# Kernel optimization log

Measured on AMD Instinct MI355X. Metric: run time of the kernel, lower is better.

## Reference

```python
import jax, jax.numpy as jnp
import numpy as np

N = 50000   # nodes
E = 600000  # edges / hyperedge incidences
D = 128     # node_in_dim
H = 128     # hidden_dim
TAU = 0.5
ALPHA = 0.5
LAM = 0.5

_PARAM_SHAPES = [('Wq0', (1, H)), ('bq0', (H,)), ('W0', (D, H)), ('b0', (H,)),
                 ('Whq0', (1, H)), ('bhq0', (H,)), ('Wh0', (D, H)), ('bh0', (H,)),
                 ('Wf0', (H, H)), ('bf0', (H,)), ('Wfh0', (H, H)), ('bfh0', (H,)),
                 ('aq0', (H,)), ('a0', (H,)), ('ahq0', (H,)), ('ah0', (H,)),
                 ('aq_', (H,)), ('a_', (H,)), ('ahq_', (H,)), ('ah_', (H,)),
                 ('Wlq', (1, H)), ('blq', (H,)), ('Wlf', (D, H)), ('blf', (H,)),
                 ('Wm1', (H, H)), ('bm1', (H,)), ('Wm2', (H, H)), ('bm2', (H,))]


def setup_inputs() -> dict:
    key = jax.random.key(0)
    ks = jax.random.split(key, 8 + len(_PARAM_SHAPES))
    inp = {}
    inp['feats'] = jax.random.normal(ks[0], (N, D), dtype=jnp.float32)
    inp['edge_index'] = jax.random.randint(ks[1], (2, E), 0, N).astype(jnp.int32)
    inp['edge_index_aug'] = jax.random.randint(ks[2], (2, E), 0, N).astype(jnp.int32)
    inp['pos'] = jax.random.randint(ks[3], (100,), 1, N).astype(jnp.int32)
    inp['q'] = 0
    for i, (nm, sh) in enumerate(_PARAM_SHAPES):
        inp[nm] = jax.random.normal(ks[4 + i], sh, dtype=jnp.float32) * 0.05
    return inp


def _forward(feats, Wq0, bq0, W0, b0, Whq0, bhq0, Wh0, bh0, Wf0, bf0, Wfh0, bfh0,
             aq0, a0, ahq0, ah0, aq_, a_, ahq_, ah_, Wlq, blq, Wlf, blf,
             Wm1, bm1, Wm2, bm2, edge_index, edge_index_aug, q, pos):
    # ---- GCNConv (PyG default: add self-loops + symmetric normalization) ----
    sl = jnp.arange(N, dtype=edge_index.dtype)
    src = jnp.concatenate([edge_index[0], sl])
    dst = jnp.concatenate([edge_index[1], sl])
    deg = jax.ops.segment_sum(jnp.ones(src.shape[0], jnp.float32), dst, num_segments=N)
    dinv = jax.lax.rsqrt(deg)  # deg >= 1 thanks to self-loops
    enorm = dinv[src] * dinv[dst]

    def gcn(x, W, b):
        xw = x @ W
        return jax.ops.segment_sum(xw[src] * enorm[:, None], dst, num_segments=N) + b

    # ---- HypergraphConv (PyG, no attention): X' = D^-1 H B^-1 H^T X W ----
    node = edge_index_aug[0]
    he = edge_index_aug[1]
    Be = jax.ops.segment_sum(jnp.ones((E,), jnp.float32), he, num_segments=N)
    Dn = jax.ops.segment_sum(jnp.ones((E,), jnp.float32), node, num_segments=N)
    Binv = jnp.where(Be > 0, 1.0 / Be, 0.0)
    Dninv = jnp.where(Dn > 0, 1.0 / Dn, 0.0)

    def hg(x, W, b):
        xw = x @ W
        me = jax.ops.segment_sum(xw[node], he, num_segments=N) * Binv[:, None]
        return jax.ops.segment_sum(me[he], node, num_segments=N) * Dninv[:, None] + b

    # ---- attention-weighted fusion of two views (softmax over 2 logits) ----
    def fuse(a, b, wa, wb):
        att = jax.nn.softmax(jnp.stack([a @ wa, b @ wb], axis=1), axis=1)  # [N,2]
        return att[:, 0:1] * a + att[:, 1:2] * b

    querys = jnp.zeros((N, 1), jnp.float32).at[q].set(1.0)
    hq = jax.nn.relu(gcn(querys, Wq0, bq0))
    h = jax.nn.relu(gcn(feats, W0, b0))
    hf = fuse(hq, h, aq0, a0)
    h_augq = jax.nn.relu(hg(querys, Whq0, bhq0))
    h_aug = jax.nn.relu(hg(feats, Wh0, bh0))
    h_augf = fuse(h_augq, h_aug, ahq0, ah0)
    querys2 = querys @ Wlq + blq
    feats2 = feats @ Wlf + blf
    hf_ = fuse(querys2, feats2, aq_, a_)
    hf = jax.nn.relu(hf + gcn(hf_, Wf0, bf0))
    hfh_ = fuse(querys2, feats2, ahq_, ah_)
    h_augf = jax.nn.relu(h_augf + hg(hfh_, Wfh0, bfh0))

    def mlp(x):
        return jax.nn.relu(x @ Wm1 + bm1) @ Wm2 + bm2

    z = mlp(hf)
    z_aug = mlp(h_augf)

    # ---- Contra loss ----
    def expcos(v, M):
        num = M @ v
        den = jnp.maximum(jnp.linalg.norm(M, axis=1) * jnp.linalg.norm(v), 1e-8)
        return jnp.exp(num / den / TAU)

    sim1 = expcos(z[q], z)
    sim_aug1 = expcos(z_aug[q], z_aug)
    sim2 = expcos(z[q], z_aug)
    sim_aug2 = expcos(z_aug[q], z)
    mask = jnp.zeros((N,), bool).at[pos].set(True).at[q].set(False)
    nmask = jnp.sum(mask).astype(jnp.float32)

    def nlm(s):  # mean over positives of -log(s_i / sum(s))
        r = jnp.log(jnp.sum(s)) - jnp.log(s)
        return jnp.sum(jnp.where(mask, r, 0.0)) / nmask

    loss_intra = 0.5 * (nlm(sim1) + nlm(sim_aug1))
    loss_inter = 0.5 * (nlm(sim2) + nlm(sim_aug2))
    z_unsup = jnp.log(jnp.sum(sim2)) - jnp.log(sim2[q])
    z_aug_unsup = jnp.log(jnp.sum(sim_aug2)) - jnp.log(sim_aug2[q])
    loss_unsup = 0.5 * z_unsup + 0.5 * z_aug_unsup
    return loss_intra + ALPHA * loss_inter + LAM * loss_unsup


def reference(feats, Wq0, bq0, W0, b0, Whq0, bhq0, Wh0, bh0, Wf0, bf0, Wfh0, bfh0,
              aq0, a0, ahq0, ah0, aq_, a_, ahq_, ah_, Wlq, blq, Wlf, blf,
              Wm1, bm1, Wm2, bm2, edge_index, edge_index_aug, q, pos):
    return _forward(feats, Wq0, bq0, W0, b0, Whq0, bhq0, Wh0, bh0, Wf0, bf0, Wfh0, bfh0,
                    aq0, a0, ahq0, ah0, aq_, a_, ahq_, ah_, Wlq, blq, Wlf, blf,
                    Wm1, bm1, Wm2, bm2, edge_index, edge_index_aug, q, pos)
```

## Files before the change

kernel.cpp:

```cpp
#include <hip/hip_runtime.h>

#define NN 50000
#define EE 600000
#define HH 128
#define TAU_INV 2.0f
#define PSZ 6250
#define CAP 48

#define BINB 512
#define BITER ((EE + BINB * 256 - 1) / (BINB * 256))
#define BUFC 240
#define QCAP 80000
#define QPAD 16
#define WSUB 32
#define SUBN 196

typedef __attribute__((ext_vector_type(8))) short short8;
typedef __attribute__((ext_vector_type(4))) float f32x4;
typedef __attribute__((ext_vector_type(2))) float floatx2;

__device__ __forceinline__ float wsum64(float v) {
#pragma unroll
  for (int m = 32; m >= 1; m >>= 1) v += __shfl_xor(v, m, 64);
  return v;
}
__device__ __forceinline__ unsigned short f2bf(float f) {
  unsigned u = __builtin_bit_cast(unsigned, f);
  u = u + 0x7FFFu + ((u >> 16) & 1u);
  return (unsigned short)(u >> 16);
}
__device__ __forceinline__ float bf2f(unsigned short h) {
  unsigned u = ((unsigned)h) << 16;
  return __builtin_bit_cast(float, u);
}
__device__ __forceinline__ unsigned char fp8_enc1(float v) {
  int p = __builtin_amdgcn_cvt_pk_fp8_f32(v, v, 0, false);
  return (unsigned char)(p & 0xFF);
}
__device__ __forceinline__ void fp8x8_dec(uint2 v, float* f) {
  floatx2 a = __builtin_amdgcn_cvt_pk_f32_fp8(v.x, false);
  floatx2 b = __builtin_amdgcn_cvt_pk_f32_fp8(v.x, true);
  floatx2 c = __builtin_amdgcn_cvt_pk_f32_fp8(v.y, false);
  floatx2 d = __builtin_amdgcn_cvt_pk_f32_fp8(v.y, true);
  f[0] = a.x; f[1] = a.y; f[2] = b.x; f[3] = b.y;
  f[4] = c.x; f[5] = c.y; f[6] = d.x; f[7] = d.y;
}
__device__ __forceinline__ uint2 fp8x8_enc(const float* f) {
  int w0 = __builtin_amdgcn_cvt_pk_fp8_f32(f[0], f[1], 0, false);
  w0 = __builtin_amdgcn_cvt_pk_fp8_f32(f[2], f[3], w0, true);
  int w1 = __builtin_amdgcn_cvt_pk_fp8_f32(f[4], f[5], 0, false);
  w1 = __builtin_amdgcn_cvt_pk_fp8_f32(f[6], f[7], w1, true);
  return make_uint2((unsigned)w0, (unsigned)w1);
}

#define LDSW 136

__global__ __launch_bounds__(256) void bin_k(const int* __restrict__ ei,
                                             const int* __restrict__ ea,
                                             int* __restrict__ qcnt,
                                             unsigned int* __restrict__ qdata) {
  __shared__ int cnt[24], base[24], pfx[25];
  __shared__ unsigned int buf[24 * BUFC];
  const int tid = threadIdx.x;
  if (tid < 24) cnt[tid] = 0;
  __syncthreads();
  for (int e = blockIdx.x * 256 + tid; e < EE; e += BINB * 256) {
    int pay0 = __builtin_nontemporal_load(ei + e);
    int k0 = __builtin_nontemporal_load(ei + EE + e);
    int pay1 = __builtin_nontemporal_load(ea + e);
    int k1 = __builtin_nontemporal_load(ea + EE + e);
    int k2 = pay1, pay2 = k1;
    int g0 = k0 / PSZ;
    int g1 = 8 + k1 / PSZ;
    int g2 = 16 + k2 / PSZ;
    int o0 = atomicAdd(&cnt[g0], 1);
    int o1 = atomicAdd(&cnt[g1], 1);
    int o2 = atomicAdd(&cnt[g2], 1);
    if (o0 < BUFC) buf[g0 * BUFC + o0] = ((unsigned)k0 << 16) | (unsigned)pay0;
    if (o1 < BUFC) buf[g1 * BUFC + o1] = ((unsigned)k1 << 16) | (unsigned)pay1;
    if (o2 < BUFC) buf[g2 * BUFC + o2] = ((unsigned)k2 << 16) | (unsigned)pay2;
  }
  __syncthreads();
  if (tid < 24) {
    int c = min(cnt[tid], BUFC);
    cnt[tid] = c;
    base[tid] = atomicAdd(&qcnt[tid * QPAD], c);
  }
  __syncthreads();
  if (tid == 0) {
    int s = 0;
#pragma unroll
    for (int g = 0; g < 24; ++g) { pfx[g] = s; s += cnt[g]; }
    pfx[24] = s;
  }
  __syncthreads();
  const int total = pfx[24];
  for (int j = tid; j < total; j += 256) {
    int lo2 = 0, hi2 = 24;
    while (lo2 + 1 < hi2) {
      int mid = (lo2 + hi2) >> 1;
      if (j >= pfx[mid]) lo2 = mid; else hi2 = mid;
    }
    int g = lo2;
    int i = j - pfx[g];
    int dq = base[g] + i;
    if (dq < QCAP) qdata[(size_t)g * QCAP + dq] = buf[g * BUFC + i];
  }
}

__global__ __launch_bounds__(256) void fillp_k(const int* __restrict__ qcnt,
                                               const unsigned int* __restrict__ qdata,
                                               int* __restrict__ cursor,
                                               unsigned short* __restrict__ slotsA,
                                               unsigned short* __restrict__ slotsB,
                                               unsigned short* __restrict__ slotsC,
                                               float* __restrict__ cntq,
                                               const int* __restrict__ qp) {
  __shared__ int cur[SUBN];
  const int w = blockIdx.x;
  const int p = w & 7;
  const int r = (w >> 3) % 3;
  const int s = w / 24;
  const int lo = p * PSZ + s * SUBN;
  const int hi = min(lo + SUBN, (p + 1) * PSZ);
  const int tid = threadIdx.x;
  if (tid < SUBN) cur[tid] = 0;
  __syncthreads();
  const int g = r * 8 + p;
  const int qlen = min(qcnt[g * QPAD], QCAP);
  const unsigned int* qd = qdata + (size_t)g * QCAP;
  unsigned short* slots = (r == 0) ? slotsA : (r == 1) ? slotsB : slotsC;
  const int q = *qp;
  auto proc = [&](unsigned int rec) {
    int key = (int)(rec >> 16);
    if (key >= lo && key < hi) {
      int pay = (int)(rec & 0xFFFFu);
      int idx = atomicAdd(&cur[key - lo], 1);
      if (idx < CAP) slots[key * CAP + idx] = (unsigned short)pay;
      if (r == 1 && pay == q) atomicAdd(&cntq[key], 1.0f);
    }
  };
  const int nv4 = qlen >> 2;
  const uint4* qd4 = (const uint4*)qd;
  int j = tid;
  for (; j + 256 < nv4; j += 512) {
    uint4 r0 = qd4[j];
    uint4 r1 = qd4[j + 256];
    proc(r0.x); proc(r0.y); proc(r0.z); proc(r0.w);
    proc(r1.x); proc(r1.y); proc(r1.z); proc(r1.w);
  }
  if (j < nv4) {
    uint4 r0 = qd4[j];
    proc(r0.x); proc(r0.y); proc(r0.z); proc(r0.w);
  }
  int i = (nv4 << 2) + tid;
  if (i < qlen) proc(qd[i]);
  __syncthreads();
  for (int k = lo + tid; k < hi; k += 256) cursor[r * NN + k] = cur[k - lo];
}

__global__ void derive_k(const int* __restrict__ cursor, float* __restrict__ dinv,
                         float* __restrict__ Binv, float* __restrict__ Dninv,
                         const int* __restrict__ pos, const int* __restrict__ qp,
                         int* __restrict__ maskI) {
  int i = blockIdx.x * 256 + threadIdx.x;
  if (i < NN) {
    dinv[i] = rsqrtf((float)(cursor[i] + 1));
    int b = cursor[NN + i];
    Binv[i] = (b > 0) ? 1.0f / (float)b : 0.0f;
    int d = cursor[2 * NN + i];
    Dninv[i] = (d > 0) ? 1.0f / (float)d : 0.0f;
  }
  if (blockIdx.x == 0) {
    int t = threadIdx.x;
    if (t < 100) maskI[pos[t]] = 1;
    __syncthreads();
    if (t == 0) maskI[*qp] = 0;
  }
}

__device__ __forceinline__ void shq_body(const int* __restrict__ ei, const int* __restrict__ ea,
                                         const int* __restrict__ qp,
                                         const float* __restrict__ dinv,
                                         const float* __restrict__ Binv,
                                         const float* __restrict__ cntq,
                                         float* __restrict__ s_hq, float* __restrict__ s_hgq,
                                         int bid) {
  int e = bid * 256 + threadIdx.x;
  if (e >= EE) return;
  int q = *qp;
  int src = __builtin_nontemporal_load(ei + e);
  if (src == q) {
    int dst = __builtin_nontemporal_load(ei + EE + e);
    atomicAdd(&s_hq[dst], dinv[q] * dinv[dst]);
  }
  int he = __builtin_nontemporal_load(ea + EE + e);
  float cq = cntq[he];
  if (cq != 0.0f) {
    int node = __builtin_nontemporal_load(ea + e);
    atomicAdd(&s_hgq[node], Binv[he] * cq);
  }
  if (e == 0) atomicAdd(&s_hq[q], dinv[q] * dinv[q]);
}

__device__ __forceinline__ void fuse2_body(const unsigned short* __restrict__ f2,
                                           const int* __restrict__ qp,
                                           const float* __restrict__ Wlq,
                                           const float* __restrict__ blq,
                                           const float* __restrict__ aq1,
                                           const float* __restrict__ a1,
                                           const float* __restrict__ aq2,
                                           const float* __restrict__ a2,
                                           unsigned short* __restrict__ out1,
                                           unsigned short* __restrict__ out2, int bid) {
  int row = bid * 4 + (threadIdx.x >> 6);
  if (row >= NN) return;
  int lane = threadIdx.x & 63;
  int c0 = lane, c1 = lane + 64;
  int q = *qp;
  float q20 = blq[c0] + ((row == q) ? Wlq[c0] : 0.f);
  float q21 = blq[c1] + ((row == q) ? Wlq[c1] : 0.f);
  float f0 = bf2f(f2[(size_t)row * 128 + c0]);
  float f1 = bf2f(f2[(size_t)row * 128 + c1]);
  float dq1 = wsum64(q20 * aq1[c0] + q21 * aq1[c1]);
  float df1 = wsum64(f0 * a1[c0] + f1 * a1[c1]);
  float dq2 = wsum64(q20 * aq2[c0] + q21 * aq2[c1]);
  float df2 = wsum64(f0 * a2[c0] + f1 * a2[c1]);
  {
    float mx = fmaxf(dq1, df1);
    float e0 = expf(dq1 - mx), e1 = expf(df1 - mx);
    float w0 = e0 / (e0 + e1), w1 = 1.f - w0;
    out1[(size_t)row * 128 + c0] = f2bf(w0 * q20 + w1 * f0);
    out1[(size_t)row * 128 + c1] = f2bf(w0 * q21 + w1 * f1);
  }
  {
    float mx = fmaxf(dq2, df2);
    float e0 = expf(dq2 - mx), e1 = expf(df2 - mx);
    float w0 = e0 / (e0 + e1), w1 = 1.f - w0;
    out2[(size_t)row * 128 + c0] = f2bf(w0 * q20 + w1 * f0);
    out2[(size_t)row * 128 + c1] = f2bf(w0 * q21 + w1 * f1);
  }
}

__global__ __launch_bounds__(256) void f2_k(const int* __restrict__ ei,
                                            const int* __restrict__ ea,
                                            const int* __restrict__ qp,
                                            const float* __restrict__ dinv,
                                            const float* __restrict__ Binv,
                                            const float* __restrict__ cntq,
                                            float* __restrict__ s_hq,
                                            float* __restrict__ s_hgq,
                                            const unsigned short* __restrict__ B6,
                                            const float* __restrict__ Wlq,
                                            const float* __restrict__ blq,
                                            const float* __restrict__ aq_,
                                            const float* __restrict__ a_,
                                            const float* __restrict__ ahq_,
                                            const float* __restrict__ ah_,
                                            unsigned short* __restrict__ B3,
                                            unsigned short* __restrict__ B4, int eb) {
  int b = blockIdx.x;
  if (b < eb)
    shq_body(ei, ea, qp, dinv, Binv, cntq, s_hq, s_hgq, b);
  else
    fuse2_body(B6, qp, Wlq, blq, aq_, a_, ahq_, ah_, B3, B4, b - eb);
}

__global__ void pack_k(const float* __restrict__ W0, const float* __restrict__ Wh0,
                       const float* __restrict__ Wlf, const float* __restrict__ Wf0,
                       const float* __restrict__ Wfh0, const float* __restrict__ Wm1,
                       const float* __restrict__ Wm2, unsigned short* __restrict__ out) {
  int tid = blockIdx.x * 256 + threadIdx.x;
  if (tid >= 7 * 2048) return;
  int mat = tid >> 11, r = tid & 2047;
  int s = r >> 9, c = (r >> 6) & 7, lane = r & 63;
  const float* W = (mat == 0) ? W0 : (mat == 1) ? Wh0 : (mat == 2) ? Wlf
                 : (mat == 3) ? Wf0 : (mat == 4) ? Wfh0 : (mat == 5) ? Wm1 : Wm2;
  int k0 = 32 * s + (lane >> 4) * 8;
  int n = 16 * c + (lane & 15);
  unsigned short* o = out + (size_t)tid * 8;
#pragma unroll
  for (int j = 0; j < 8; ++j) o[j] = f2bf(W[(k0 + j) * 128 + n]);
}

template <bool BIAS, bool RELU, int OM>
__device__ __forceinline__ void gemm_core(const unsigned short* As, const short8* Wp,
                                          const float* bias, void* outv, int r0, int nrows,
                                          int tid) {
  const int wave = tid >> 6, lane = tid & 63;
  const int quad = lane >> 4, l15 = lane & 15;
  const int rw = r0 + wave * 16;
  f32x4 acc[8];
#pragma unroll
  for (int c = 0; c < 8; ++c) acc[c] = (f32x4){0.f, 0.f, 0.f, 0.f};
#pragma unroll
  for (int s = 0; s < 4; ++s) {
    short8 a = *(const short8*)&As[(wave * 16 + l15) * LDSW + s * 32 + quad * 8];
#pragma unroll
    for (int c = 0; c < 8; ++c) {
      short8 b = Wp[(s * 8 + c) * 64 + lane];
      acc[c] = __builtin_amdgcn_mfma_f32_16x16x32_bf16(a, b, acc[c], 0, 0, 0);
    }
  }
#pragma unroll
  for (int c = 0; c < 8; ++c) {
    int col = c * 16 + l15;
    float bv = BIAS ? bias[col] : 0.f;
#pragma unroll
    for (int r = 0; r < 4; ++r) {
      int grow = rw + quad * 4 + r;
      if (grow < nrows) {
        float v = acc[c][r] + bv;
        if (RELU) v = fmaxf(v, 0.f);
        if (OM == 2)
          ((unsigned char*)outv)[(size_t)grow * 256 + col] = fp8_enc1(v);
        else if (OM == 1)
          ((unsigned short*)outv)[(size_t)grow * 128 + col] = f2bf(v);
        else
          ((float*)outv)[(size_t)grow * 128 + col] = v;
      }
    }
  }
}

__device__ __forceinline__ void stage_bf16(const unsigned short* A, unsigned short* As,
                                           int r0, int nrows, int tid) {
#pragma unroll
  for (int t = 0; t < 4; ++t) {
    int v = t * 256 + tid;
    int row = v >> 4, cc = v & 15;
    int gr = r0 + row;
    uint4 val = make_uint4(0, 0, 0, 0);
    if (gr < nrows) val = ((const uint4*)A)[(size_t)gr * 16 + cc];
    *(uint4*)&As[row * LDSW + cc * 8] = val;
  }
}

template <bool BIAS, bool RELU, int OM>
__global__ __launch_bounds__(256) void gemm2_mfma(const unsigned short* __restrict__ A0,
                                                  const unsigned short* __restrict__ A1,
                                                  const short8* __restrict__ Wp0,
                                                  const short8* __restrict__ Wp1,
                                                  const float* __restrict__ b0,
                                                  const float* __restrict__ b1,
                                                  void* __restrict__ o0, void* __restrict__ o1,
                                                  int nrows, int nblk) {
  __shared__ unsigned short As[64 * LDSW];
  int b = blockIdx.x;
  const unsigned short* A = A0;
  const short8* Wp = Wp0;
  const float* bias = b0;
  void* o = o0;
  if (b >= nblk) {
    b -= nblk; A = A1; Wp = Wp1; bias = b1; o = o1;
  }
  const int r0 = b * 64;
  stage_bf16(A, As, r0, nrows, threadIdx.x);
  __syncthreads();
  gemm_core<BIAS, RELU, OM>(As, Wp, bias, o, r0, nrows, threadIdx.x);
}

__global__ __launch_bounds__(256) void gemm3_mfma(const float* __restrict__ A,
                                                  const short8* __restrict__ Wp,
                                                  const float* __restrict__ bias2,
                                                  unsigned char* __restrict__ p1,
                                                  unsigned char* __restrict__ p2,
                                                  unsigned short* __restrict__ out2,
                                                  int nrows) {
  __shared__ unsigned short As[64 * LDSW];
  const int tid = threadIdx.x;
  const int r0 = blockIdx.x * 64;
#pragma unroll
  for (int t = 0; t < 8; ++t) {
    int v = t * 256 + tid;
    int row = v >> 5, c4 = v & 31;
    int gr = r0 + row;
    f32x4 val = (f32x4){0.f, 0.f, 0.f, 0.f};
    if (gr < nrows) {
      const f32x4* src = (const f32x4*)A + (size_t)gr * 32 + c4;
      val = __builtin_nontemporal_load(src);
    }
    ushort4 o;
    o.x = f2bf(val.x); o.y = f2bf(val.y); o.z = f2bf(val.z); o.w = f2bf(val.w);
    *(ushort4*)&As[row * LDSW + c4 * 4] = o;
  }
  __syncthreads();
  const int wave = tid >> 6, lane = tid & 63;
  const int quad = lane >> 4, l15 = lane & 15;
  const int rw = r0 + wave * 16;
  f32x4 acc[3][8];
#pragma unroll
  for (int m = 0; m < 3; ++m)
#pragma unroll
    for (int c = 0; c < 8; ++c) acc[m][c] = (f32x4){0.f, 0.f, 0.f, 0.f};
#pragma unroll
  for (int s = 0; s < 4; ++s) {
    short8 a = *(const short8*)&As[(wave * 16 + l15) * LDSW + s * 32 + quad * 8];
#pragma unroll
    for (int m = 0; m < 3; ++m)
#pragma unroll
      for (int c = 0; c < 8; ++c) {
        short8 bb = Wp[(size_t)m * 2048 + (s * 8 + c) * 64 + lane];
        acc[m][c] = __builtin_amdgcn_mfma_f32_16x16x32_bf16(a, bb, acc[m][c], 0, 0, 0);
      }
  }
#pragma unroll
  for (int c = 0; c < 8; ++c) {
    int col = c * 16 + l15;
    float bv = bias2[col];
#pragma unroll
    for (int r = 0; r < 4; ++r) {
      int grow = rw + quad * 4 + r;
      if (grow < nrows) {
        p1[(size_t)grow * 256 + col] = fp8_enc1(acc[0][c][r]);
        p2[(size_t)grow * 256 + col] = fp8_enc1(acc[1][c][r]);
        out2[(size_t)grow * 128 + col] = f2bf(acc[2][c][r] + bv);
      }
    }
  }
}

template <int MODE, bool OUTFP8>
__device__ __forceinline__ void gpair_body(const uint2* __restrict__ xp,
                                           unsigned short* __restrict__ y1,
                                           unsigned short* __restrict__ y2,
                                           uint2* __restrict__ yp,
                                           const int* __restrict__ cnt,
                                           const unsigned short* __restrict__ slots,
                                           const float* __restrict__ wv, int blk) {
  int node = blk * 8 + (threadIdx.x >> 5);
  if (node >= NN) return;
  int l = threadIdx.x & 31;
  int st = node * CAP;
  int n = min(cnt[node], CAP);
  float acc[8];
#pragma unroll
  for (int i = 0; i < 8; ++i) acc[i] = 0.f;
  int p = 0;
  for (; p + 4 <= n; p += 4) {
    ushort4 s4 = *(const ushort4*)&slots[st + p];
    uint2 v0 = xp[(size_t)s4.x * 32 + l];
    uint2 v1 = xp[(size_t)s4.y * 32 + l];
    uint2 v2 = xp[(size_t)s4.z * 32 + l];
    uint2 v3 = xp[(size_t)s4.w * 32 + l];
    float f[8];
    if (MODE == 0) {
      float w0 = wv[s4.x], w1 = wv[s4.y], w2 = wv[s4.z], w3 = wv[s4.w];
      fp8x8_dec(v0, f);
#pragma unroll
      for (int i = 0; i < 8; ++i) acc[i] = fmaf(w0, f[i], acc[i]);
      fp8x8_dec(v1, f);
#pragma unroll
      for (int i = 0; i < 8; ++i) acc[i] = fmaf(w1, f[i], acc[i]);
      fp8x8_dec(v2, f);
#pragma unroll
      for (int i = 0; i < 8; ++i) acc[i] = fmaf(w2, f[i], acc[i]);
      fp8x8_dec(v3, f);
#pragma unroll
      for (int i = 0; i < 8; ++i) acc[i] = fmaf(w3, f[i], acc[i]);
    } else {
      fp8x8_dec(v0, f);
#pragma unroll
      for (int i = 0; i < 8; ++i) acc[i] += f[i];
      fp8x8_dec(v1, f);
#pragma unroll
      for (int i = 0; i < 8; ++i) acc[i] += f[i];
      fp8x8_dec(v2, f);
#pragma unroll
      for (int i = 0; i < 8; ++i) acc[i] += f[i];
      fp8x8_dec(v3, f);
#pragma unroll
      for (int i = 0; i < 8; ++i) acc[i] += f[i];
    }
  }
  for (; p < n; ++p) {
    int s = slots[st + p];
    uint2 v = xp[(size_t)s * 32 + l];
    float f[8];
    fp8x8_dec(v, f);
    if (MODE == 0) {
      float w = wv[s];
#pragma unroll
      for (int i = 0; i < 8; ++i) acc[i] = fmaf(w, f[i], acc[i]);
    } else {
#pragma unroll
      for (int i = 0; i < 8; ++i) acc[i] += f[i];
    }
  }
  float sc = wv[node];
  if (MODE == 0) {
    uint2 v = xp[(size_t)node * 32 + l];
    float f[8];
    fp8x8_dec(v, f);
#pragma unroll
    for (int i = 0; i < 8; ++i) acc[i] = sc * fmaf(sc, f[i], acc[i]);
  } else {
#pragma unroll
    for (int i = 0; i < 8; ++i) acc[i] *= sc;
  }
  if (OUTFP8) {
    yp[(size_t)node * 32 + l] = fp8x8_enc(acc);
  } else {
    unsigned short* y = (l < 16) ? y1 : y2;
    int cg = l & 15;
    uint4 o;
    o.x = ((unsigned)f2bf(acc[1]) << 16) | f2bf(acc[0]);
    o.y = ((unsigned)f2bf(acc[3]) << 16) | f2bf(acc[2]);
    o.z = ((unsigned)f2bf(acc[5]) << 16) | f2bf(acc[4]);
    o.w = ((unsigned)f2bf(acc[7]) << 16) | f2bf(acc[6]);
    *(uint4*)&y[(size_t)node * 128 + cg * 8] = o;
  }
}

__global__ void dgather12_k(const uint2* __restrict__ xp1, unsigned short* __restrict__ y1a,
                            unsigned short* __restrict__ y1b, const uint2* __restrict__ xp2,
                            uint2* __restrict__ yp3, const int* __restrict__ cursor,
                            const unsigned short* __restrict__ slotsA,
                            const unsigned short* __restrict__ slotsB,
                            const float* __restrict__ dinv, const float* __restrict__ Binv,
                            int nblk) {
  int b = blockIdx.x;
  if (b < nblk)
    gpair_body<0, false>(xp1, y1a, y1b, nullptr, cursor, slotsA, dinv, b);
  else
    gpair_body<1, true>(xp2, nullptr, nullptr, yp3, cursor + NN, slotsB, Binv, b - nblk);
}

__global__ void dgather3_k(const uint2* __restrict__ xp, unsigned short* __restrict__ y1,
                           unsigned short* __restrict__ y2, const int* __restrict__ cursor,
                           const unsigned short* __restrict__ slotsC,
                           const float* __restrict__ wv) {
  gpair_body<1, false>(xp, y1, y2, nullptr, cursor + 2 * NN, slotsC, wv, blockIdx.x);
}

__device__ __forceinline__ void fuse_add_body(const unsigned short* __restrict__ g,
                                              const unsigned short* __restrict__ gr,
                                              const float* __restrict__ svec,
                                              const float* __restrict__ dscale,
                                              const float* __restrict__ Wq,
                                              const float* __restrict__ bq,
                                              const float* __restrict__ bm,
                                              const float* __restrict__ aq,
                                              const float* __restrict__ am,
                                              const float* __restrict__ bres,
                                              unsigned short* __restrict__ out, int blk) {
  int row = blk * 4 + (threadIdx.x >> 6);
  if (row >= NN) return;
  int lane = threadIdx.x & 63;
  int c0 = lane, c1 = lane + 64;
  float s = svec[row];
  if (dscale) s *= dscale[row];
  float hq0 = fmaxf(fmaf(s, Wq[c0], bq[c0]), 0.f);
  float hq1 = fmaxf(fmaf(s, Wq[c1], bq[c1]), 0.f);
  float h0 = fmaxf(bf2f(g[(size_t)row * 128 + c0]) + bm[c0], 0.f);
  float h1 = fmaxf(bf2f(g[(size_t)row * 128 + c1]) + bm[c1], 0.f);
  float dq = wsum64(hq0 * aq[c0] + hq1 * aq[c1]);
  float dm = wsum64(h0 * am[c0] + h1 * am[c1]);
  float mx = fmaxf(dq, dm);
  float e0 = expf(dq - mx), e1 = expf(dm - mx);
  float w0 = e0 / (e0 + e1), w1 = 1.f - w0;
  float r0 = fmaxf(w0 * hq0 + w1 * h0 + bf2f(gr[(size_t)row * 128 + c0]) + bres[c0], 0.f);
  float r1 = fmaxf(w0 * hq1 + w1 * h1 + bf2f(gr[(size_t)row * 128 + c1]) + bres[c1], 0.f);
  out[(size_t)row * 128 + c0] = f2bf(r0);
  out[(size_t)row * 128 + c1] = f2bf(r1);
}

__global__ void fuse_add2_k(const unsigned short* gA, const unsigned short* grA,
                            const float* svA, const float* dsA, const float* WqA,
                            const float* bqA, const float* bmA, const float* aqA,
                            const float* amA, const float* brA, unsigned short* outA,
                            const unsigned short* gB, const unsigned short* grB,
                            const float* svB, const float* dsB, const float* WqB,
                            const float* bqB, const float* bmB, const float* aqB,
                            const float* amB, const float* brB, unsigned short* outB,
                            int nblk) {
  int b = blockIdx.x;
  if (b < nblk)
    fuse_add_body(gA, grA, svA, dsA, WqA, bqA, bmA, aqA, amA, brA, outA, b);
  else
    fuse_add_body(gB, grB, svB, dsB, WqB, bqB, bmB, aqB, amB, brB, outB, b - nblk);
}

__global__ void sim_k(const unsigned short* __restrict__ z,
                      const unsigned short* __restrict__ za, const int* __restrict__ qp,
                      float4* __restrict__ simbuf, float* __restrict__ scal_out) {
  int row = blockIdx.x * 4 + (threadIdx.x >> 6);
  if (row >= NN) return;
  int lane = threadIdx.x & 63;
  int c0 = lane, c1 = lane + 64;
  int q = *qp;
  float zi0 = bf2f(z[(size_t)row * 128 + c0]), zi1 = bf2f(z[(size_t)row * 128 + c1]);
  float zai0 = bf2f(za[(size_t)row * 128 + c0]), zai1 = bf2f(za[(size_t)row * 128 + c1]);
  float zq0 = bf2f(z[(size_t)q * 128 + c0]), zq1 = bf2f(z[(size_t)q * 128 + c1]);
  float zaq0 = bf2f(za[(size_t)q * 128 + c0]), zaq1 = bf2f(za[(size_t)q * 128 + c1]);
  float nzi = wsum64(zi0 * zi0 + zi1 * zi1);
  float nzai = wsum64(zai0 * zai0 + zai1 * zai1);
  float nzq = wsum64(zq0 * zq0 + zq1 * zq1);
  float nzaq = wsum64(zaq0 * zaq0 + zaq1 * zaq1);
  float d1 = wsum64(zi0 * zq0 + zi1 * zq1);
  float d2 = wsum64(zai0 * zaq0 + zai1 * zaq1);
  float d3 = wsum64(zai0 * zq0 + zai1 * zq1);
  float d4 = wsum64(zi0 * zaq0 + zi1 * zaq1);
  if (lane == 0) {
    float ni = sqrtf(nzi), nai = sqrtf(nzai);
    float nq = sqrtf(nzq), naq = sqrtf(nzaq);
    float c1_ = d1 / fmaxf(ni * nq, 1e-8f) * TAU_INV;
    float ca1 = d2 / fmaxf(nai * naq, 1e-8f) * TAU_INV;
    float c2_ = d3 / fmaxf(nai * nq, 1e-8f) * TAU_INV;
    float ca2 = d4 / fmaxf(ni * naq, 1e-8f) * TAU_INV;
    simbuf[row] = make_float4(c1_, ca1, c2_, ca2);
    if (row == q) {
      scal_out[9] = c2_;
      scal_out[10] = ca2;
    }
  }
}

__global__ __launch_bounds__(256) void reduce_sim_k(const float4* __restrict__ simbuf,
                                                    const int* __restrict__ maskI,
                                                    float* __restrict__ scal) {
  float acc[9];
#pragma unroll
  for (int i = 0; i < 9; ++i) acc[i] = 0.f;
  for (int row = blockIdx.x * 256 + threadIdx.x; row < NN; row += gridDim.x * 256) {
    float4 v = simbuf[row];
    acc[0] += expf(v.x);
    acc[1] += expf(v.y);
    acc[2] += expf(v.z);
    acc[3] += expf(v.w);
    if (maskI[row]) {
      acc[4] += v.x; acc[5] += v.y; acc[6] += v.z; acc[7] += v.w;
      acc[8] += 1.0f;
    }
  }
  __shared__ float s[9][4];
  int lane = threadIdx.x & 63, wv = threadIdx.x >> 6;
#pragma unroll
  for (int i = 0; i < 9; ++i) {
    float r = wsum64(acc[i]);
    if (lane == 0) s[i][wv] = r;
  }
  __syncthreads();
  if (threadIdx.x < 9) {
    float r = s[threadIdx.x][0] + s[threadIdx.x][1] + s[threadIdx.x][2] + s[threadIdx.x][3];
    atomicAdd(&scal[threadIdx.x], r);
  }
}

__global__ void final_k(const float* __restrict__ scal, float* __restrict__ out) {
  if (threadIdx.x != 0 || blockIdx.x != 0) return;
  float S1 = scal[0], Sa1 = scal[1], S2 = scal[2], Sa2 = scal[3];
  float L1 = scal[4], La1 = scal[5], L2 = scal[6], La2 = scal[7];
  float NM = scal[8], Q2 = scal[9], Qa2 = scal[10];
  float intra = 0.5f * ((logf(S1) - L1 / NM) + (logf(Sa1) - La1 / NM));
  float inter = 0.5f * ((logf(S2) - L2 / NM) + (logf(Sa2) - La2 / NM));
  float unsup = 0.5f * (logf(S2) - Q2) + 0.5f * (logf(Sa2) - Qa2);
  out[0] = intra + 0.5f * inter + 0.5f * unsup;
}

extern "C" void kernel_launch(void* const* d_in, const int* in_sizes, int n_in,
                              void* d_out, int out_size, void* d_ws, size_t ws_size,
                              hipStream_t stream) {
  const float* feats = (const float*)d_in[0];
  const int* ei = (const int*)d_in[1];
  const int* ea = (const int*)d_in[2];
  const int* pos = (const int*)d_in[3];
  const int* qp = (const int*)d_in[4];
  const float* Wq0 = (const float*)d_in[5];
  const float* bq0 = (const float*)d_in[6];
  const float* W0 = (const float*)d_in[7];
  const float* b0 = (const float*)d_in[8];
  const float* Whq0 = (const float*)d_in[9];
  const float* bhq0 = (const float*)d_in[10];
  const float* Wh0 = (const float*)d_in[11];
  const float* bh0 = (const float*)d_in[12];
  const float* Wf0 = (const float*)d_in[13];
  const float* bf0 = (const float*)d_in[14];
  const float* Wfh0 = (const float*)d_in[15];
  const float* bfh0 = (const float*)d_in[16];
  const float* aq0 = (const float*)d_in[17];
  const float* a0 = (const float*)d_in[18];
  const float* ahq0 = (const float*)d_in[19];
  const float* ah0 = (const float*)d_in[20];
  const float* aq_ = (const float*)d_in[21];
  const float* a_ = (const float*)d_in[22];
  const float* ahq_ = (const float*)d_in[23];
  const float* ah_ = (const float*)d_in[24];
  const float* Wlq = (const float*)d_in[25];
  const float* blq = (const float*)d_in[26];
  const float* Wlf = (const float*)d_in[27];
  const float* blf = (const float*)d_in[28];
  const float* Wm1 = (const float*)d_in[29];
  const float* bm1 = (const float*)d_in[30];
  const float* Wm2 = (const float*)d_in[31];
  const float* bm2 = (const float*)d_in[32];

  char* ws = (char*)d_ws;
  size_t off = 0;
  auto take = [&](size_t bytes) -> void* {
    void* p = ws + off;
    off = (off + bytes + 255) & ~(size_t)255;
    return p;
  };
  int* cursor3 = (int*)take(3 * NN * 4);
  int* maskI = (int*)take(NN * 4);
  float* s_hq = (float*)take(NN * 4);
  float* cntq = (float*)take(NN * 4);
  float* s_hgq = (float*)take(NN * 4);
  float* scal = (float*)take(64 * 4);
  int* qcnt = (int*)take(24 * QPAD * 4);
  size_t zero_end = off;
  unsigned short* slotsA = (unsigned short*)take((size_t)NN * CAP * 2);
  unsigned short* slotsB = (unsigned short*)take((size_t)NN * CAP * 2);
  unsigned short* slotsC = (unsigned short*)take((size_t)NN * CAP * 2);
  unsigned int* qdata = (unsigned int*)take((size_t)24 * QCAP * 4);
  float* dinv = (float*)take(NN * 4);
  float* Binv = (float*)take(NN * 4);
  float* Dninv = (float*)take(NN * 4);
  float4* simbuf = (float4*)take((size_t)NN * 16);
  unsigned short* Wpack = (unsigned short*)take((size_t)7 * 16384 * 2);
  const size_t BFSZ = (size_t)NN * HH * 2;
  unsigned short* B0 = (unsigned short*)take(BFSZ);
  unsigned short* B1 = (unsigned short*)take(BFSZ);
  unsigned short* B2 = (unsigned short*)take(BFSZ);
  unsigned short* B3 = (unsigned short*)take(BFSZ);
  unsigned short* B4 = (unsigned short*)take(BFSZ);
  unsigned short* B5 = (unsigned short*)take(BFSZ);
  unsigned short* B6 = (unsigned short*)take(BFSZ);
  unsigned char* P1 = (unsigned char*)take((size_t)NN * 256);
  unsigned char* P2 = (unsigned char*)take((size_t)NN * 256);
  unsigned char* P3 = (unsigned char*)take((size_t)NN * 256);

  const int NB = (NN + 255) / 256;
  const int EB = (EE + 255) / 256;
  const int GMB = (NN + 63) / 64;
  const int GTB = (NN + 7) / 8;
  const int RB = (NN + 3) / 4;
  const short8* Wp = (const short8*)Wpack;

  hipMemsetAsync(d_ws, 0, zero_end, stream);
  pack_k<<<(7 * 2048 + 255) / 256, 256, 0, stream>>>(W0, Wh0, Wlf, Wf0, Wfh0, Wm1, Wm2,
                                                     Wpack);
  bin_k<<<BINB, 256, 0, stream>>>(ei, ea, qcnt, qdata);
  fillp_k<<<24 * WSUB, 256, 0, stream>>>(qcnt, qdata, cursor3, slotsA, slotsB, slotsC,
                                         cntq, qp);
  gemm3_mfma<<<GMB, 256, 0, stream>>>(feats, Wp, blf, P1, P2, B6, NN);
  derive_k<<<NB, 256, 0, stream>>>(cursor3, dinv, Binv, Dninv, pos, qp, maskI);
  f2_k<<<EB + RB, 256, 0, stream>>>(ei, ea, qp, dinv, Binv, cntq, s_hq, s_hgq, B6, Wlq,
                                    blq, aq_, a_, ahq_, ah_, B3, B4, EB);
  gemm2_mfma<false, false, 2><<<2 * GMB, 256, 0, stream>>>(
      B3, B4, Wp + (size_t)3 * 2048, Wp + (size_t)4 * 2048, nullptr, nullptr, P1 + 128,
      P2 + 128, NN, GMB);
  dgather12_k<<<2 * GTB, 256, 0, stream>>>((const uint2*)P1, B0, B1, (const uint2*)P2,
                                           (uint2*)P3, cursor3, slotsA, slotsB, dinv, Binv,
                                           GTB);
  dgather3_k<<<GTB, 256, 0, stream>>>((const uint2*)P3, B2, B5, cursor3, slotsC, Dninv);
  fuse_add2_k<<<2 * RB, 256, 0, stream>>>(
      B0, B1, s_hq, nullptr, Wq0, bq0, b0, aq0, a0, bf0, B3,
      B2, B5, s_hgq, Dninv, Whq0, bhq0, bh0, ahq0, ah0, bfh0, B4, RB);
  gemm2_mfma<true, true, 1><<<2 * GMB, 256, 0, stream>>>(
      B3, B4, Wp + (size_t)5 * 2048, Wp + (size_t)5 * 2048, bm1, bm1, B0, B1, NN, GMB);
  gemm2_mfma<true, false, 1><<<2 * GMB, 256, 0, stream>>>(
      B0, B1, Wp + (size_t)6 * 2048, Wp + (size_t)6 * 2048, bm2, bm2, B2, B5, NN, GMB);
  sim_k<<<RB, 256, 0, stream>>>(B2, B5, qp, simbuf, scal);
  reduce_sim_k<<<64, 256, 0, stream>>>(simbuf, maskI, scal);
  final_k<<<1, 64, 0, stream>>>(scal, (float*)d_out);
}
```

Before: 465.3 us.

## Stage GEMM epilogues through LDS for coalesced stores; split gemm3 across column halves

The GEMM epilogues now write their results into shared memory first and then emit 16-byte row-contiguous global stores, replacing scattered 1- and 2-byte per-lane stores. gemm3_mfma is split so each block computes half the output columns, which doubles the grid and halves the accumulator registers, at the cost of each row tile of feats being loaded and converted twice. The nontemporal load hint on feats is also dropped. The change adds extra barriers and LDS traffic per block.

```diff
diff --git a/kernel.cpp b/kernel.cpp
--- a/kernel.cpp
+++ b/kernel.cpp
@@ -8,7 +8,6 @@
 #define CAP 48
 
 #define BINB 512
-#define BITER ((EE + BINB * 256 - 1) / (BINB * 256))
 #define BUFC 240
 #define QCAP 80000
 #define QPAD 16
@@ -284,12 +283,11 @@
 }
 
 template <bool BIAS, bool RELU, int OM>
-__device__ __forceinline__ void gemm_core(const unsigned short* As, const short8* Wp,
+__device__ __forceinline__ void gemm_core(unsigned short* As, const short8* Wp,
                                           const float* bias, void* outv, int r0, int nrows,
                                           int tid) {
   const int wave = tid >> 6, lane = tid & 63;
   const int quad = lane >> 4, l15 = lane & 15;
-  const int rw = r0 + wave * 16;
   f32x4 acc[8];
 #pragma unroll
   for (int c = 0; c < 8; ++c) acc[c] = (f32x4){0.f, 0.f, 0.f, 0.f};
@@ -302,23 +300,52 @@
       acc[c] = __builtin_amdgcn_mfma_f32_16x16x32_bf16(a, b, acc[c], 0, 0, 0);
     }
   }
-#pragma unroll
-  for (int c = 0; c < 8; ++c) {
-    int col = c * 16 + l15;
-    float bv = BIAS ? bias[col] : 0.f;
-#pragma unroll
-    for (int r = 0; r < 4; ++r) {
-      int grow = rw + quad * 4 + r;
-      if (grow < nrows) {
+  __syncthreads();
+  const int rwl = wave * 16 + quad * 4;
+  if (OM == 2) {
+    unsigned char* l8 = (unsigned char*)As;
+#pragma unroll
+    for (int c = 0; c < 8; ++c) {
+      int col = c * 16 + l15;
+      float bv = BIAS ? bias[col] : 0.f;
+#pragma unroll
+      for (int r = 0; r < 4; ++r) {
         float v = acc[c][r] + bv;
         if (RELU) v = fmaxf(v, 0.f);
-        if (OM == 2)
-          ((unsigned char*)outv)[(size_t)grow * 256 + col] = fp8_enc1(v);
-        else if (OM == 1)
-          ((unsigned short*)outv)[(size_t)grow * 128 + col] = f2bf(v);
-        else
-          ((float*)outv)[(size_t)grow * 128 + col] = v;
+        l8[(rwl + r) * 128 + col] = fp8_enc1(v);
       }
+    }
+    __syncthreads();
+#pragma unroll
+    for (int t = 0; t < 2; ++t) {
+      int idx = (t * 256 + tid) * 16;
+      int row = idx >> 7, off = idx & 127;
+      int grow = r0 + row;
+      if (grow < nrows)
+        *(uint4*)&((unsigned char*)outv)[(size_t)grow * 256 + off] = *(uint4*)&l8[idx];
+    }
+  } else {
+    unsigned short* l16 = As;
+#pragma unroll
+    for (int c = 0; c < 8; ++c) {
+      int col = c * 16 + l15;
+      float bv = BIAS ? bias[col] : 0.f;
+#pragma unroll
+      for (int r = 0; r < 4; ++r) {
+        float v = acc[c][r] + bv;
+        if (RELU) v = fmaxf(v, 0.f);
+        l16[(rwl + r) * 128 + col] = f2bf(v);
+      }
+    }
+    __syncthreads();
+#pragma unroll
+    for (int t = 0; t < 4; ++t) {
+      int idx = (t * 256 + tid) * 16;
+      int row = idx >> 8, off = idx & 255;
+      int grow = r0 + row;
+      if (grow < nrows)
+        *(uint4*)&((unsigned char*)outv)[(size_t)grow * 256 + off] =
+            *(uint4*)&((unsigned char*)l16)[idx];
     }
   }
 }
@@ -369,17 +396,15 @@
                                                   int nrows) {
   __shared__ unsigned short As[64 * LDSW];
   const int tid = threadIdx.x;
-  const int r0 = blockIdx.x * 64;
+  const int bh = blockIdx.x & 1;
+  const int r0 = (blockIdx.x >> 1) * 64;
 #pragma unroll
   for (int t = 0; t < 8; ++t) {
     int v = t * 256 + tid;
     int row = v >> 5, c4 = v & 31;
     int gr = r0 + row;
     f32x4 val = (f32x4){0.f, 0.f, 0.f, 0.f};
-    if (gr < nrows) {
-      const f32x4* src = (const f32x4*)A + (size_t)gr * 32 + c4;
-      val = __builtin_nontemporal_load(src);
-    }
+    if (gr < nrows) val = ((const f32x4*)A)[(size_t)gr * 32 + c4];
     ushort4 o;
     o.x = f2bf(val.x); o.y = f2bf(val.y); o.z = f2bf(val.z); o.w = f2bf(val.w);
     *(ushort4*)&As[row * LDSW + c4 * 4] = o;
@@ -387,36 +412,57 @@
   __syncthreads();
   const int wave = tid >> 6, lane = tid & 63;
   const int quad = lane >> 4, l15 = lane & 15;
-  const int rw = r0 + wave * 16;
-  f32x4 acc[3][8];
+  f32x4 acc[3][4];
 #pragma unroll
   for (int m = 0; m < 3; ++m)
 #pragma unroll
-    for (int c = 0; c < 8; ++c) acc[m][c] = (f32x4){0.f, 0.f, 0.f, 0.f};
+    for (int c = 0; c < 4; ++c) acc[m][c] = (f32x4){0.f, 0.f, 0.f, 0.f};
 #pragma unroll
   for (int s = 0; s < 4; ++s) {
     short8 a = *(const short8*)&As[(wave * 16 + l15) * LDSW + s * 32 + quad * 8];
 #pragma unroll
     for (int m = 0; m < 3; ++m)
 #pragma unroll
-      for (int c = 0; c < 8; ++c) {
-        short8 bb = Wp[(size_t)m * 2048 + (s * 8 + c) * 64 + lane];
+      for (int c = 0; c < 4; ++c) {
+        short8 bb = Wp[(size_t)m * 2048 + (s * 8 + bh * 4 + c) * 64 + lane];
         acc[m][c] = __builtin_amdgcn_mfma_f32_16x16x32_bf16(a, bb, acc[m][c], 0, 0, 0);
       }
   }
-#pragma unroll
-  for (int c = 0; c < 8; ++c) {
-    int col = c * 16 + l15;
-    float bv = bias2[col];
+  __syncthreads();
+  unsigned char* l8a = (unsigned char*)As;
+  unsigned char* l8b = l8a + 4096;
+  unsigned short* l16 = (unsigned short*)(l8a + 8192);
+  const int rwl = wave * 16 + quad * 4;
+#pragma unroll
+  for (int c = 0; c < 4; ++c) {
+    int coll = c * 16 + l15;
+    float bv = bias2[(bh * 4 + c) * 16 + l15];
 #pragma unroll
     for (int r = 0; r < 4; ++r) {
-      int grow = rw + quad * 4 + r;
-      if (grow < nrows) {
-        p1[(size_t)grow * 256 + col] = fp8_enc1(acc[0][c][r]);
-        p2[(size_t)grow * 256 + col] = fp8_enc1(acc[1][c][r]);
-        out2[(size_t)grow * 128 + col] = f2bf(acc[2][c][r] + bv);
-      }
-    }
+      int lrow = rwl + r;
+      l8a[lrow * 64 + coll] = fp8_enc1(acc[0][c][r]);
+      l8b[lrow * 64 + coll] = fp8_enc1(acc[1][c][r]);
+      l16[lrow * 64 + coll] = f2bf(acc[2][c][r] + bv);
+    }
+  }
+  __syncthreads();
+  {
+    int idx = tid * 16;
+    int row = idx >> 6, off = idx & 63;
+    int grow = r0 + row;
+    if (grow < nrows) {
+      *(uint4*)&p1[(size_t)grow * 256 + bh * 64 + off] = *(uint4*)&l8a[idx];
+      *(uint4*)&p2[(size_t)grow * 256 + bh * 64 + off] = *(uint4*)&l8b[idx];
+    }
+  }
+#pragma unroll
+  for (int t = 0; t < 2; ++t) {
+    int idx = (t * 256 + tid) * 16;
+    int row = idx >> 7, off = idx & 127;
+    int grow = r0 + row;
+    if (grow < nrows)
+      *(uint4*)&((unsigned char*)out2)[(size_t)grow * 256 + bh * 128 + off] =
+          *(uint4*)&((unsigned char*)l16)[idx];
   }
 }
 
@@ -744,7 +790,7 @@
   bin_k<<<BINB, 256, 0, stream>>>(ei, ea, qcnt, qdata);
   fillp_k<<<24 * WSUB, 256, 0, stream>>>(qcnt, qdata, cursor3, slotsA, slotsB, slotsC,
                                          cntq, qp);
-  gemm3_mfma<<<GMB, 256, 0, stream>>>(feats, Wp, blf, P1, P2, B6, NN);
+  gemm3_mfma<<<2 * GMB, 256, 0, stream>>>(feats, Wp, blf, P1, P2, B6, NN);
   derive_k<<<NB, 256, 0, stream>>>(cursor3, dinv, Binv, Dninv, pos, qp, maskI);
   f2_k<<<EB + RB, 256, 0, stream>>>(ei, ea, qp, dinv, Binv, cntq, s_hq, s_hgq, B6, Wlq,
                                     blq, aq_, a_, ahq_, ah_, B3, B4, EB);
```

New measurement: 426.4 us. -8.4%, faster.
